# Performance work log

Measured on AMD Instinct MI355X. Metric: run time of the kernel, lower is better.

## Reference

```python
import jax, jax.numpy as jnp
import numpy as np

N_HEAD = 16


def _rope_tables(T, head_dim, dtype):
    # RotaryEmbedding buffers: freqs = outer(t, inv_freq), half-dim tables [T, head_dim//2]
    inv_freq = 1.0 / (10000.0 ** (jnp.arange(0, head_dim, 2, dtype=jnp.float32) / head_dim))
    freqs = jnp.arange(T, dtype=jnp.float32)[:, None] * inv_freq[None, :]
    return jnp.cos(freqs).astype(dtype), jnp.sin(freqs).astype(dtype)


def _apply_rotary(x, cos, sin):
    # x: [B,H,T,D]; cos/sin: [T,D//2] broadcast over B,H
    d = x.shape[-1] // 2
    x1, x2 = x[..., :d], x[..., d:]
    return jnp.concatenate([x1 * cos - x2 * sin, x2 * cos + x1 * sin], axis=-1)


def setup_inputs() -> dict:
    key = jax.random.key(0)
    k1, k2, k3 = jax.random.split(key, 3)
    B, T, C = 2, 2048, 2048
    x = jax.random.normal(k1, (B, T, C), dtype=jnp.float32)
    Wqkv = jax.random.normal(k2, (C, 3 * C), dtype=jnp.float32) * (1.0 / np.sqrt(C))
    Wproj = jax.random.normal(k3, (C, C), dtype=jnp.float32) * (1.0 / np.sqrt(C))
    return {"x": x, "Wqkv": Wqkv, "Wproj": Wproj}


def reference(x, Wqkv, Wproj):
    B, T, C = x.shape
    H = N_HEAD
    D = C // H
    qkv = (x @ Wqkv).reshape(B, T, 3, H, D)
    q, k, v = qkv[:, :, 0], qkv[:, :, 1], qkv[:, :, 2]  # [B,T,H,D]
    q = jnp.transpose(q, (0, 2, 1, 3))  # [B,H,T,D]
    k = jnp.transpose(k, (0, 2, 1, 3))
    v = jnp.transpose(v, (0, 2, 1, 3))
    cos, sin = _rope_tables(T, D, x.dtype)
    q = _apply_rotary(q, cos, sin)
    k = _apply_rotary(k, cos, sin)
    scale = 1.0 / np.sqrt(D)
    scores = jnp.einsum('bhqd,bhkd->bhqk', q, k) * scale
    causal = jnp.tril(jnp.ones((T, T), dtype=bool))
    scores = jnp.where(causal, scores, jnp.finfo(scores.dtype).min)
    attn = jax.nn.softmax(scores, axis=-1)
    out = jnp.einsum('bhqk,bhkd->bhqd', attn, v)
    out = jnp.transpose(out, (0, 2, 1, 3)).reshape(B, T, C)
    return out @ Wproj
```

## Files before the change

### kernel.cpp

```cpp
#include <hip/hip_runtime.h>
#include <hip/hip_bf16.h>

typedef short s16b;
using bf16x4 = __attribute__((ext_vector_type(4))) short;
using bf16x8 = __attribute__((ext_vector_type(8))) short;
using f32x4  = __attribute__((ext_vector_type(4))) float;

#define DEVINL __device__ __forceinline__

DEVINL float bf2f(short u) {
    union { float f; unsigned u; } x;
    x.u = ((unsigned)(unsigned short)u) << 16;
    return x.f;
}
DEVINL short f2bf(float f) {
    unsigned u = __builtin_bit_cast(unsigned, f);
    u += 0x7FFFu + ((u >> 16) & 1u);
    return (short)(u >> 16);
}

DEVINL f32x4 mfma16(bf16x8 a, bf16x8 b, f32x4 c) {
    return __builtin_amdgcn_mfma_f32_16x16x32_bf16(a, b, c, 0, 0, 0);
}

DEVINL void gload_lds16(const void* g, void* lds_uniform) {
    __builtin_amdgcn_global_load_lds(
        (const __attribute__((address_space(1))) char*)(const char*)g,
        (__attribute__((address_space(3))) char*)(char*)lds_uniform, 16, 0, 0);
}

DEVINL int perm32(int k) {
    return ((k >> 2) & 3) * 8 + ((k >> 4) & 1) * 4 + (k & 3);
}

DEVINL bf16x8 lds128(const s16b* base, int row, int ks, int g) {
    const char* p = (const char*)base + row * 128 + ((((ks << 2) + g) ^ (row & 7)) << 4);
    return *(const bf16x8*)p;
}
DEVINL bf16x8 lds256(const s16b* base, int row, int ds, int g) {
    const char* p = (const char*)base + row * 256 + ((((ds << 2) + g) ^ (row & 7)) << 4);
    return *(const bf16x8*)p;
}

__global__ void k_tables(float* __restrict__ ctab, float* __restrict__ stab) {
    int idx = blockIdx.x * 256 + threadIdx.x;
    int i = idx & 63, t = idx >> 6;
    float inv = powf(10000.0f, -(float)i * (1.0f / 64.0f));
    float fr = (float)t * inv;
    ctab[idx] = cosf(fr);
    stab[idx] = sinf(fr);
}

__global__ void k_cvt_x(const float* __restrict__ x, s16b* __restrict__ xb) {
    int idx = blockIdx.x * 256 + threadIdx.x;
    int p = idx * 4;
    int row = p >> 11, pc = p & 2047;
    int grp = pc >> 5, sp = pc & 31;
    int c = sp >> 3, half = (sp >> 2) & 1;
    int ksrc = grp * 32 + half * 16 + c * 4;
    float4 v = *(const float4*)(x + (size_t)row * 2048 + ksrc);
    bf16x4 o;
    o[0] = f2bf(v.x); o[1] = f2bf(v.y); o[2] = f2bf(v.z); o[3] = f2bf(v.w);
    *(bf16x4*)(xb + (size_t)row * 2048 + pc) = o;
}

__global__ void k_tcvt(const float* __restrict__ in, s16b* __restrict__ out, int R, int C) {
    __shared__ float tile[32][33];
    int tx = threadIdx.x & 31, ty = threadIdx.x >> 5;
    int c0 = blockIdx.x * 32, r0 = blockIdx.y * 32;
#pragma unroll
    for (int kk = 0; kk < 4; ++kk) {
        int r = ty + kk * 8;
        tile[r][tx] = in[(size_t)(r0 + r) * C + c0 + tx];
    }
    __syncthreads();
#pragma unroll
    for (int kk = 0; kk < 4; ++kk) {
        int r = ty + kk * 8;
        out[(size_t)(c0 + r) * R + r0 + perm32(tx)] = f2bf(tile[tx][r]);
    }
}

#define STG_TILE(DB, KB)                                                       \
  gload_lds16(srcA + (KB), lds + (DB) * 16384 + tid16);                        \
  gload_lds16(srcA + 262144 + (KB), lds + (DB) * 16384 + 8192 + tid16);        \
  gload_lds16(srcB + (KB), lds + 49152 + (DB) * 32768 + tid16);                \
  gload_lds16(srcB + 262144 + (KB), lds + 49152 + (DB) * 32768 + 8192 + tid16);\
  gload_lds16(srcB + 524288 + (KB), lds + 49152 + (DB) * 32768 + 16384 + tid16);\
  gload_lds16(srcB + 786432 + (KB), lds + 49152 + (DB) * 32768 + 24576 + tid16);

#define AF_READ(B, KS)                                                         \
    _Pragma("unroll")                                                          \
    for (int fi = 0; fi < 4; ++fi) {                                           \
      int row = (fi >> 1) * 64 + wm * 32 + (fi & 1) * 16 + r15;                \
      af[fi] = *(const bf16x8*)(lds + (B) * 16384 + row * 128                  \
               + ((((KS) * 4 + g) ^ (row & 7)) << 4));                         \
    }
#define BF_READ(B, KS)                                                         \
    _Pragma("unroll")                                                          \
    for (int fj = 0; fj < 4; ++fj) {                                           \
      int row = (fj >> 1) * 128 + wn * 32 + (fj & 1) * 16 + r15;               \
      bfr[fj] = *(const bf16x8*)(lds + 49152 + (B) * 32768 + row * 128         \
                + ((((KS) * 4 + g) ^ (row & 7)) << 4));                        \
    }

#define MFMAS                                                                  \
  __builtin_amdgcn_s_setprio(1);                                               \
  _Pragma("unroll")                                                            \
  for (int fi = 0; fi < 4; ++fi)                                               \
    _Pragma("unroll")                                                          \
    for (int fj = 0; fj < 4; ++fj)                                             \
      acc[fi][fj] = mfma16(af[fi], bfr[fj], acc[fi][fj]);                      \
  __builtin_amdgcn_s_setprio(0);

#define DO_TILE(B, B2, KB, DOSTG, WN)                                          \
  {                                                                            \
    AF_READ(B, 0) BF_READ(B, 0)                                                \
    if (DOSTG) { STG_TILE(B2, (KB) + 256) }                                    \
    MFMAS                                                                      \
    AF_READ(B, 1) BF_READ(B, 1)                                                \
    if ((WN) == 6) { asm volatile("s_waitcnt vmcnt(6)" ::: "memory");          \
                     __builtin_amdgcn_sched_barrier(0); }                      \
    else if ((WN) == 0) { asm volatile("s_waitcnt vmcnt(0)" ::: "memory");     \
                     __builtin_amdgcn_sched_barrier(0); }                      \
    MFMAS                                                                      \
    __builtin_amdgcn_s_barrier();                                              \
    asm volatile("" ::: "memory");                                             \
    __builtin_amdgcn_sched_barrier(0);                                         \
  }

#define GEMM3_MAINLOOP(A_, B_)                                                 \
    __shared__ __attribute__((aligned(16))) char lds[147456];                  \
    const int tid = threadIdx.x;                                               \
    const int lane = tid & 63, wave = tid >> 6;                                \
    const int g = lane >> 4, r15 = lane & 15;                                  \
    const int wm = wave >> 2, wn = wave & 3;                                   \
    const int tid16 = tid << 4;                                                \
    const int rowL = tid16 >> 7;                                               \
    const int swzL = ((((tid16 >> 4) & 7) ^ (rowL & 7)) << 4);                 \
    const char* srcA = (const char*)(A_) + (size_t)(bm + rowL) * 4096 + swzL;  \
    const char* srcB = (const char*)(B_) + (size_t)(bn + rowL) * 4096 + swzL;  \
    f32x4 acc[4][4] = {};                                                      \
    bf16x8 af[4], bfr[4];                                                      \
    STG_TILE(0, 0) STG_TILE(1, 128)                                            \
    asm volatile("s_waitcnt vmcnt(6)" ::: "memory");                           \
    __builtin_amdgcn_sched_barrier(0);                                         \
    __builtin_amdgcn_s_barrier();                                              \
    asm volatile("" ::: "memory");                                             \
    for (int t3 = 0; t3 < 10; ++t3) {                                          \
        const int kb = t3 * 384;                                               \
        DO_TILE(0, 2, kb, 1, 6)                                                \
        DO_TILE(1, 0, kb + 128, 1, 6)                                          \
        DO_TILE(2, 1, kb + 256, 1, 6)                                          \
    }                                                                          \
    DO_TILE(0, 2, 3840, 0, 0)                                                  \
    DO_TILE(1, 0, 3968, 0, -1)

__global__ __launch_bounds__(512) void k_gemm_qkv(
    const s16b* __restrict__ A, const s16b* __restrict__ Bt,
    s16b* __restrict__ Qb, s16b* __restrict__ Kb, s16b* __restrict__ Vt) {
    const int bid = blockIdx.x;
    const int xcd = bid & 7, local = bid >> 3;
    const int rr_ = local >> 5, w = local & 31;
    const int bm = ((xcd & 3) * 8 + (w >> 2)) * 128;
    const int bn = ((xcd >> 2) * 12 + rr_ * 4 + (w & 3)) * 256;
    GEMM3_MAINLOOP(A, Bt)
#pragma unroll
    for (int i = 0; i < 4; ++i) {
        int m0 = bm + (i >> 1) * 64 + wm * 32 + (i & 1) * 16 + 4 * g;
        int b = m0 >> 11, t0 = m0 & 2047;
#pragma unroll
        for (int j = 0; j < 4; ++j) {
            int n = bn + (j >> 1) * 128 + wn * 32 + (j & 1) * 16 + r15;
            int which = n >> 11;
            int h = (n >> 7) & 15, d = n & 127;
            size_t bh = (size_t)(b * 16 + h);
            if (which == 0) {
                size_t base = (bh * 2048 + t0) * 128 + d;
#pragma unroll
                for (int e = 0; e < 4; ++e) Qb[base + (size_t)e * 128] = f2bf(acc[i][j][e]);
            } else if (which == 1) {
                size_t base = (bh * 2048 + t0) * 128 + d;
#pragma unroll
                for (int e = 0; e < 4; ++e) Kb[base + (size_t)e * 128] = f2bf(acc[i][j][e]);
            } else {
                int pt = (t0 & ~31) + perm32(t0 & 31);
                size_t base = (bh * 128 + d) * 2048 + pt;
                bf16x4 pk;
#pragma unroll
                for (int e = 0; e < 4; ++e) pk[e] = f2bf(acc[i][j][e]);
                *(bf16x4*)(Vt + base) = pk;
            }
        }
    }
}

__global__ __launch_bounds__(512) void k_gemm_proj(
    const s16b* __restrict__ A, const s16b* __restrict__ Bt, float* __restrict__ Co) {
    const int bid = blockIdx.x;
    const int xcd = bid & 7, local = bid >> 3;
    const int bm = (xcd * 4 + (local & 3)) * 128;
    const int bn = (local >> 2) * 256;
    GEMM3_MAINLOOP(A, Bt)
#pragma unroll
    for (int i = 0; i < 4; ++i) {
        int m0 = bm + (i >> 1) * 64 + wm * 32 + (i & 1) * 16 + 4 * g;
#pragma unroll
        for (int j = 0; j < 4; ++j) {
            int n = bn + (j >> 1) * 128 + wn * 32 + (j & 1) * 16 + r15;
#pragma unroll
            for (int e = 0; e < 4; ++e) Co[(size_t)(m0 + e) * 2048 + n] = acc[i][j][e];
        }
    }
}

__global__ void k_rope(s16b* __restrict__ Qb, const s16b* __restrict__ Kb,
                       s16b* __restrict__ Kp,
                       const float* __restrict__ ctab, const float* __restrict__ stab) {
    int idx = blockIdx.x * 256 + threadIdx.x;
    int i4 = idx & 15;
    int t = (idx >> 4) & 2047;
    int bh = (idx >> 15) & 31;
    int which = idx >> 20;
    int d = i4 * 4;
    const float* cp = ctab + t * 64 + d;
    const float* sp = stab + t * 64 + d;
    size_t rowoff = ((size_t)bh * 2048 + t) * 128;
    if (which == 0) {
        s16b* P = Qb + rowoff;
        bf16x4 a = *(bf16x4*)(P + d);
        bf16x4 bv = *(bf16x4*)(P + d + 64);
        bf16x4 ra, rb;
#pragma unroll
        for (int e = 0; e < 4; ++e) {
            float c = cp[e], s = sp[e];
            float x1 = bf2f(a[e]), x2 = bf2f(bv[e]);
            ra[e] = f2bf(x1 * c - x2 * s);
            rb[e] = f2bf(x2 * c + x1 * s);
        }
        *(bf16x4*)(P + d) = ra;
        *(bf16x4*)(P + d + 64) = rb;
    } else {
        const s16b* Pi = Kb + rowoff;
        s16b* Po = Kp + rowoff;
        bf16x4 a = *(const bf16x4*)(Pi + d);
        bf16x4 bv = *(const bf16x4*)(Pi + d + 64);
        bf16x4 ra, rb;
#pragma unroll
        for (int e = 0; e < 4; ++e) {
            float c = cp[e], s = sp[e];
            float x1 = bf2f(a[e]), x2 = bf2f(bv[e]);
            ra[e] = f2bf(x1 * c - x2 * s);
            rb[e] = f2bf(x2 * c + x1 * s);
        }
        int d2 = d + 64;
        int pd  = (d  & ~31) + perm32(d  & 31);
        int pd2 = (d2 & ~31) + perm32(d2 & 31);
        *(bf16x4*)(Po + pd) = ra;
        *(bf16x4*)(Po + pd2) = rb;
    }
}

__global__ __launch_bounds__(256) void k_attn(
    const s16b* __restrict__ Qb, const s16b* __restrict__ Kp,
    const s16b* __restrict__ Vt, s16b* __restrict__ AO) {
    __shared__ alignas(16) s16b Ks[64 * 128];
    __shared__ alignas(16) s16b Vs[128 * 64];
    const int tid = threadIdx.x;
    const int lane = tid & 63, wave = tid >> 6;
    const int g = lane >> 4, r15 = lane & 15;
    const int bh = blockIdx.x, qt = 15 - blockIdx.y;
    const int q0 = qt * 128 + wave * 32;
    const s16b* Qg = Qb + (size_t)bh * 2048 * 128;
    const char* Kg = (const char*)(Kp + (size_t)bh * 2048 * 128);
    const char* Vg = (const char*)(Vt + (size_t)bh * 128 * 2048);

    bf16x8 qf[2][4];
#pragma unroll
    for (int qs = 0; qs < 2; ++qs)
#pragma unroll
        for (int ds = 0; ds < 4; ++ds) {
            const s16b* p = Qg + (size_t)(q0 + qs * 16 + r15) * 128 + ds * 32 + 4 * g;
            bf16x4 lo = *(const bf16x4*)p;
            bf16x4 hi = *(const bf16x4*)(p + 16);
            qf[qs][ds] = __builtin_shufflevector(lo, hi, 0, 1, 2, 3, 4, 5, 6, 7);
        }

    f32x4 ot[8][2] = {};
    float m_s[2] = {-3e38f, -3e38f};
    float l_s[2] = {0.f, 0.f};
    const float scale = 0.0883883476483184f;

    const int ktiles = qt * 2 + 2;
    for (int kt = 0; kt < ktiles; ++kt) {
        const int k0 = kt * 64;
        __syncthreads();
#pragma unroll
        for (int rr = 0; rr < 4; ++rr) {
            int uo = (rr * 256 + wave * 64) * 16;
            int o = uo + lane * 16;
            {
                int row = o >> 8, sl = (o >> 4) & 15;
                int sg = (sl ^ (row & 7)) << 4;
                gload_lds16(Kg + (size_t)(k0 + row) * 256 + sg, (char*)Ks + uo);
            }
            {
                int row = o >> 7, sl = (o >> 4) & 7;
                int sg = (sl ^ (row & 7)) << 4;
                gload_lds16(Vg + (size_t)row * 4096 + (size_t)k0 * 2 + sg, (char*)Vs + uo);
            }
        }
        __syncthreads();

        if (k0 <= q0 + 31) {
            f32x4 st[4][2] = {};
            __builtin_amdgcn_s_setprio(1);
#pragma unroll
            for (int ds = 0; ds < 4; ++ds) {
#pragma unroll
                for (int ks = 0; ks < 4; ++ks) {
                    bf16x8 kf = lds256(Ks, ks * 16 + r15, ds, g);
#pragma unroll
                    for (int qs = 0; qs < 2; ++qs)
                        st[ks][qs] = mfma16(kf, qf[qs][ds], st[ks][qs]);
                }
            }
            __builtin_amdgcn_s_setprio(0);
#pragma unroll
            for (int ks = 0; ks < 4; ++ks)
#pragma unroll
                for (int qs = 0; qs < 2; ++qs)
#pragma unroll
                    for (int e = 0; e < 4; ++e) {
                        int kk = k0 + ks * 16 + 4 * g + e;
                        int qq = q0 + qs * 16 + r15;
                        float s = st[ks][qs][e] * scale;
                        st[ks][qs][e] = (kk <= qq) ? s : -3e38f;
                    }
            float sf[2];
#pragma unroll
            for (int qs = 0; qs < 2; ++qs) {
                float mx = -3e38f;
#pragma unroll
                for (int ks = 0; ks < 4; ++ks)
#pragma unroll
                    for (int e = 0; e < 4; ++e) mx = fmaxf(mx, st[ks][qs][e]);
                mx = fmaxf(mx, __shfl_xor(mx, 16));
                mx = fmaxf(mx, __shfl_xor(mx, 32));
                float mn = fmaxf(m_s[qs], mx);
                sf[qs] = __expf(m_s[qs] - mn);
                m_s[qs] = mn;
                float sum = 0.f;
#pragma unroll
                for (int ks = 0; ks < 4; ++ks)
#pragma unroll
                    for (int e = 0; e < 4; ++e) {
                        float p = __expf(st[ks][qs][e] - mn);
                        st[ks][qs][e] = p;
                        sum += p;
                    }
                sum += __shfl_xor(sum, 16);
                sum += __shfl_xor(sum, 32);
                l_s[qs] = l_s[qs] * sf[qs] + sum;
            }
            bf16x8 pb[2][2];
#pragma unroll
            for (int k2 = 0; k2 < 2; ++k2)
#pragma unroll
                for (int qs = 0; qs < 2; ++qs) {
                    bf16x8 f;
#pragma unroll
                    for (int jj = 0; jj < 8; ++jj)
                        f[jj] = f2bf(st[2 * k2 + (jj >> 2)][qs][jj & 3]);
                    pb[k2][qs] = f;
                }
#pragma unroll
            for (int d8 = 0; d8 < 8; ++d8)
#pragma unroll
                for (int qs = 0; qs < 2; ++qs)
#pragma unroll
                    for (int e = 0; e < 4; ++e) ot[d8][qs][e] *= sf[qs];
            __builtin_amdgcn_s_setprio(1);
#pragma unroll
            for (int k2 = 0; k2 < 2; ++k2)
#pragma unroll
                for (int d8 = 0; d8 < 8; ++d8) {
                    bf16x8 vf = lds128(Vs, d8 * 16 + r15, k2, g);
#pragma unroll
                    for (int qs = 0; qs < 2; ++qs)
                        ot[d8][qs] = mfma16(vf, pb[k2][qs], ot[d8][qs]);
                }
            __builtin_amdgcn_s_setprio(0);
        }
    }
    int b = bh >> 4, h = bh & 15;
#pragma unroll
    for (int qs = 0; qs < 2; ++qs) {
        float inv = 1.0f / l_s[qs];
        int q = q0 + qs * 16 + r15;
#pragma unroll
        for (int d8 = 0; d8 < 8; ++d8) {
            bf16x4 pk;
#pragma unroll
            for (int e = 0; e < 4; ++e) pk[e] = f2bf(ot[d8][qs][e] * inv);
            size_t off = ((size_t)(b * 2048 + q)) * 2048
                       + h * 128 + (d8 >> 1) * 32 + g * 8 + (d8 & 1) * 4;
            *(bf16x4*)(AO + off) = pk;
        }
    }
}

extern "C" void kernel_launch(void* const* d_in, const int* in_sizes, int n_in,
                              void* d_out, int out_size, void* d_ws, size_t ws_size,
                              hipStream_t stream) {
    const float* x = (const float*)d_in[0];
    const float* Wqkv = (const float*)d_in[1];
    const float* Wproj = (const float*)d_in[2];
    float* out = (float*)d_out;

    char* ws = (char*)d_ws;
    float* ctab = (float*)ws;
    float* stab = ctab + 2048 * 64;
    size_t off = 1048576;
    s16b* xb = (s16b*)(ws + off); off += 16777216;
    s16b* wqkvt = (s16b*)(ws + off); off += 25165824;
    s16b* wprojt = (s16b*)(ws + off); off += 8388608;
    s16b* Qb = (s16b*)(ws + off); off += 16777216;
    s16b* Kb = (s16b*)(ws + off); off += 16777216;
    s16b* Vt = (s16b*)(ws + off); off += 16777216;
    s16b* AO = xb;
    s16b* Kp = wqkvt;

    k_tables<<<dim3(512), dim3(256), 0, stream>>>(ctab, stab);
    k_cvt_x<<<dim3(8192), dim3(256), 0, stream>>>(x, xb);
    k_tcvt<<<dim3(192, 64), dim3(256), 0, stream>>>(Wqkv, wqkvt, 2048, 6144);
    k_tcvt<<<dim3(64, 64), dim3(256), 0, stream>>>(Wproj, wprojt, 2048, 2048);
    k_gemm_qkv<<<dim3(768), dim3(512), 0, stream>>>(xb, wqkvt, Qb, Kb, Vt);
    k_rope<<<dim3(8192), dim3(256), 0, stream>>>(Qb, Kb, Kp, ctab, stab);
    k_attn<<<dim3(32, 16), dim3(256), 0, stream>>>(Qb, Kp, Vt, AO);
    k_gemm_proj<<<dim3(256), dim3(512), 0, stream>>>(AO, wprojt, out);
}
```

Baseline: 273.1 us.

## Split GEMM tiles into four interleaved phases and stage Q/K epilogue through LDS

The GEMM main loop is restructured into four phases per K-tile. Each phase loads half of the B fragments, issues one third of the next tile's global-to-LDS loads, and runs eight MFMAs between barriers, so memory traffic is spread more evenly across the compute. The QKV epilogue for the Q and K outputs now writes bf16 results into swizzled LDS and then stores them as 16-byte rows, replacing scattered 2-byte global stores. The extra barriers per tile add synchronization overhead, and the epilogue reuses the main-loop LDS buffer.

```diff
diff --git a/kernel.cpp b/kernel.cpp
--- a/kernel.cpp
+++ b/kernel.cpp
@@ -81,13 +81,15 @@
     }
 }
 
-#define STG_TILE(DB, KB)                                                       \
+#define STG_B01(DB, KB)                                                        \
+  gload_lds16(srcB + (KB), lds + 49152 + (DB) * 32768 + tid16);                \
+  gload_lds16(srcB + 262144 + (KB), lds + 49152 + (DB) * 32768 + 8192 + tid16);
+#define STG_B23(DB, KB)                                                        \
+  gload_lds16(srcB + 524288 + (KB), lds + 49152 + (DB) * 32768 + 16384 + tid16); \
+  gload_lds16(srcB + 786432 + (KB), lds + 49152 + (DB) * 32768 + 24576 + tid16);
+#define STG_A01(DB, KB)                                                        \
   gload_lds16(srcA + (KB), lds + (DB) * 16384 + tid16);                        \
-  gload_lds16(srcA + 262144 + (KB), lds + (DB) * 16384 + 8192 + tid16);        \
-  gload_lds16(srcB + (KB), lds + 49152 + (DB) * 32768 + tid16);                \
-  gload_lds16(srcB + 262144 + (KB), lds + 49152 + (DB) * 32768 + 8192 + tid16);\
-  gload_lds16(srcB + 524288 + (KB), lds + 49152 + (DB) * 32768 + 16384 + tid16);\
-  gload_lds16(srcB + 786432 + (KB), lds + 49152 + (DB) * 32768 + 24576 + tid16);
+  gload_lds16(srcA + 262144 + (KB), lds + (DB) * 16384 + 8192 + tid16);
 
 #define AF_READ(B, KS)                                                         \
     _Pragma("unroll")                                                          \
@@ -96,38 +98,40 @@
       af[fi] = *(const bf16x8*)(lds + (B) * 16384 + row * 128                  \
                + ((((KS) * 4 + g) ^ (row & 7)) << 4));                         \
     }
-#define BF_READ(B, KS)                                                         \
+
+#define PH4(B, KH, JH, STGC, WN)                                               \
+  {                                                                            \
+    if ((JH) == 0) { AF_READ(B, KH) }                                          \
     _Pragma("unroll")                                                          \
-    for (int fj = 0; fj < 4; ++fj) {                                           \
-      int row = (fj >> 1) * 128 + wn * 32 + (fj & 1) * 16 + r15;               \
+    for (int fj = 0; fj < 2; ++fj) {                                           \
+      int row = (JH) * 128 + wn * 32 + fj * 16 + r15;                          \
       bfr[fj] = *(const bf16x8*)(lds + 49152 + (B) * 32768 + row * 128         \
-                + ((((KS) * 4 + g) ^ (row & 7)) << 4));                        \
-    }
-
-#define MFMAS                                                                  \
-  __builtin_amdgcn_s_setprio(1);                                               \
-  _Pragma("unroll")                                                            \
-  for (int fi = 0; fi < 4; ++fi)                                               \
-    _Pragma("unroll")                                                          \
-    for (int fj = 0; fj < 4; ++fj)                                             \
-      acc[fi][fj] = mfma16(af[fi], bfr[fj], acc[fi][fj]);                      \
-  __builtin_amdgcn_s_setprio(0);
-
-#define DO_TILE(B, B2, KB, DOSTG, WN)                                          \
-  {                                                                            \
-    AF_READ(B, 0) BF_READ(B, 0)                                                \
-    if (DOSTG) { STG_TILE(B2, (KB) + 256) }                                    \
-    MFMAS                                                                      \
-    AF_READ(B, 1) BF_READ(B, 1)                                                \
+                + ((((KH) * 4 + g) ^ (row & 7)) << 4));                        \
+    }                                                                          \
+    STGC                                                                       \
     if ((WN) == 6) { asm volatile("s_waitcnt vmcnt(6)" ::: "memory");          \
                      __builtin_amdgcn_sched_barrier(0); }                      \
     else if ((WN) == 0) { asm volatile("s_waitcnt vmcnt(0)" ::: "memory");     \
                      __builtin_amdgcn_sched_barrier(0); }                      \
-    MFMAS                                                                      \
     __builtin_amdgcn_s_barrier();                                              \
-    asm volatile("" ::: "memory");                                             \
+    asm volatile("s_waitcnt lgkmcnt(0)" ::: "memory");                         \
+    __builtin_amdgcn_sched_barrier(0);                                         \
+    __builtin_amdgcn_s_setprio(1);                                             \
+    _Pragma("unroll")                                                          \
+    for (int fi = 0; fi < 4; ++fi)                                             \
+      _Pragma("unroll")                                                        \
+      for (int fj = 0; fj < 2; ++fj)                                           \
+        acc[fi][(JH) * 2 + fj] = mfma16(af[fi], bfr[fj], acc[fi][(JH) * 2 + fj]); \
+    __builtin_amdgcn_s_setprio(0);                                             \
+    __builtin_amdgcn_s_barrier();                                              \
     __builtin_amdgcn_sched_barrier(0);                                         \
   }
+
+#define DO_TILE3(B, S1, S2, S3, WNL)                                           \
+    PH4(B, 0, 0, S1, -1)                                                       \
+    PH4(B, 0, 1, S2, -1)                                                       \
+    PH4(B, 1, 0, S3, -1)                                                       \
+    PH4(B, 1, 1, , WNL)
 
 #define GEMM3_MAINLOOP(A_, B_)                                                 \
     __shared__ __attribute__((aligned(16))) char lds[147456];                  \
@@ -141,20 +145,21 @@
     const char* srcA = (const char*)(A_) + (size_t)(bm + rowL) * 4096 + swzL;  \
     const char* srcB = (const char*)(B_) + (size_t)(bn + rowL) * 4096 + swzL;  \
     f32x4 acc[4][4] = {};                                                      \
-    bf16x8 af[4], bfr[4];                                                      \
-    STG_TILE(0, 0) STG_TILE(1, 128)                                            \
+    bf16x8 af[4], bfr[2];                                                      \
+    STG_B01(0, 0) STG_A01(0, 0) STG_B23(0, 0)                                  \
+    STG_B01(1, 128) STG_A01(1, 128) STG_B23(1, 128)                            \
     asm volatile("s_waitcnt vmcnt(6)" ::: "memory");                           \
     __builtin_amdgcn_sched_barrier(0);                                         \
     __builtin_amdgcn_s_barrier();                                              \
-    asm volatile("" ::: "memory");                                             \
     for (int t3 = 0; t3 < 10; ++t3) {                                          \
-        const int kb = t3 * 384;                                               \
-        DO_TILE(0, 2, kb, 1, 6)                                                \
-        DO_TILE(1, 0, kb + 128, 1, 6)                                          \
-        DO_TILE(2, 1, kb + 256, 1, 6)                                          \
+        const int kb2 = (3 * t3 + 2) * 128;                                    \
+        const int kb3 = kb2 + 128, kb4 = kb2 + 256;                            \
+        DO_TILE3(0, STG_B01(2, kb2), STG_A01(2, kb2), STG_B23(2, kb2), 6)      \
+        DO_TILE3(1, STG_B01(0, kb3), STG_A01(0, kb3), STG_B23(0, kb3), 6)      \
+        DO_TILE3(2, STG_B01(1, kb4), STG_A01(1, kb4), STG_B23(1, kb4), 6)      \
     }                                                                          \
-    DO_TILE(0, 2, 3840, 0, 0)                                                  \
-    DO_TILE(1, 0, 3968, 0, -1)
+    DO_TILE3(0, , , , 0)                                                       \
+    DO_TILE3(1, , , , -1)
 
 __global__ __launch_bounds__(512) void k_gemm_qkv(
     const s16b* __restrict__ A, const s16b* __restrict__ Bt,
@@ -165,25 +170,48 @@
     const int bm = ((xcd & 3) * 8 + (w >> 2)) * 128;
     const int bn = ((xcd >> 2) * 12 + rr_ * 4 + (w & 3)) * 256;
     GEMM3_MAINLOOP(A, Bt)
-#pragma unroll
-    for (int i = 0; i < 4; ++i) {
-        int m0 = bm + (i >> 1) * 64 + wm * 32 + (i & 1) * 16 + 4 * g;
-        int b = m0 >> 11, t0 = m0 & 2047;
-#pragma unroll
-        for (int j = 0; j < 4; ++j) {
-            int n = bn + (j >> 1) * 128 + wn * 32 + (j & 1) * 16 + r15;
-            int which = n >> 11;
-            int h = (n >> 7) & 15, d = n & 127;
-            size_t bh = (size_t)(b * 16 + h);
-            if (which == 0) {
-                size_t base = (bh * 2048 + t0) * 128 + d;
-#pragma unroll
-                for (int e = 0; e < 4; ++e) Qb[base + (size_t)e * 128] = f2bf(acc[i][j][e]);
-            } else if (which == 1) {
-                size_t base = (bh * 2048 + t0) * 128 + d;
-#pragma unroll
-                for (int e = 0; e < 4; ++e) Kb[base + (size_t)e * 128] = f2bf(acc[i][j][e]);
-            } else {
+    const int which = bn >> 11;
+    if (which < 2) {
+        s16b* dst = which ? Kb : Qb;
+        char* sml = (char*)lds;
+#pragma unroll
+        for (int i = 0; i < 4; ++i) {
+#pragma unroll
+            for (int j = 0; j < 4; ++j) {
+                int mb0 = (i >> 1) * 64 + wm * 32 + (i & 1) * 16 + 4 * g;
+                int nn = (j >> 1) * 128 + wn * 32 + (j & 1) * 16 + r15;
+#pragma unroll
+                for (int e = 0; e < 4; ++e) {
+                    int mm = mb0 + e;
+                    *(s16b*)(sml + mm * 528 + ((nn * 2) ^ ((mm & 3) << 5))) =
+                        f2bf(acc[i][j][e]);
+                }
+            }
+        }
+        __syncthreads();
+        const int mrow = tid >> 2, c4 = tid & 3;
+        const int bb = bm >> 11;
+        const int tt = (bm & 2047) + mrow;
+        const char* srow = sml + mrow * 528;
+        const int sw = (mrow & 3) << 5;
+#pragma unroll
+        for (int k = 0; k < 8; ++k) {
+            int lc = c4 + 4 * k;
+            bf16x8 v = *(const bf16x8*)(srow + ((lc * 16) ^ sw));
+            int ng = bn + lc * 8;
+            int h = (ng >> 7) & 15, d = ng & 127;
+            *(bf16x8*)(dst + ((size_t)(bb * 16 + h) * 2048 + tt) * 128 + d) = v;
+        }
+    } else {
+#pragma unroll
+        for (int i = 0; i < 4; ++i) {
+            int m0 = bm + (i >> 1) * 64 + wm * 32 + (i & 1) * 16 + 4 * g;
+            int b = m0 >> 11, t0 = m0 & 2047;
+#pragma unroll
+            for (int j = 0; j < 4; ++j) {
+                int n = bn + (j >> 1) * 128 + wn * 32 + (j & 1) * 16 + r15;
+                int h = (n >> 7) & 15, d = n & 127;
+                size_t bh = (size_t)(b * 16 + h);
                 int pt = (t0 & ~31) + perm32(t0 & 31);
                 size_t base = (bh * 128 + d) * 2048 + pt;
                 bf16x4 pk;
```

After: 270.2 us. About the same (-1.1%).
